# Kernel tuning notes

Measured on AMD Instinct MI355X. Metric: run time of the kernel, lower is better.

Reference implementation:

```python
import jax, jax.numpy as jnp
import numpy as np

# ---- config (matches init_kwargs) ----
L_LEVELS = 10          # int(log(8192/16)/log(2)) + 1
LEVEL_DIM = 4
BASE_RES = 16
LOG2_T = 21
BOUND = 2.0            # contract() output bound
DENSITY_BIAS = -1.0
RGB_PADDING = 0.001
DEG_VIEW = 4
PRIME1 = np.uint32(2654435761)
PRIME2 = np.uint32(805459861)


def _grid_meta():
    # torch-ngp GridEncoder layout: per-level scale = base*2^l - 1 (per_level_scale=2),
    # resolution = base*2^l, params = min(2^21, (res+1)^3) rounded up to multiple of 8.
    offsets, scales, res_list, sizes = [0], [], [], []
    for l in range(L_LEVELS):
        res = BASE_RES * (2 ** l)
        scales.append(float(res - 1))
        n = min(2 ** LOG2_T, (res + 1) ** 3)
        n = int(np.ceil(n / 8) * 8)
        res_list.append(res)
        sizes.append(n)
        offsets.append(offsets[-1] + n)
    return scales, res_list, sizes, offsets

GRID_SCALES, GRID_RES, GRID_SIZES, GRID_OFFSETS = _grid_meta()
TOTAL_PARAMS = GRID_OFFSETS[-1]  # 14995560
CORNERS = np.array([[(c >> d) & 1 for d in range(3)] for c in range(8)], dtype=np.int32)


def contract(x):
    # mipnerf360 contraction, output in [-2, 2]
    eps = jnp.finfo(x.dtype).eps
    x_mag_sq = jnp.maximum(eps, jnp.sum(x * x, axis=-1, keepdims=True))
    return jnp.where(x_mag_sq <= 1.0, x, ((2.0 * jnp.sqrt(x_mag_sq) - 1.0) / x_mag_sq) * x)


def pos_enc(x):
    # coord.pos_enc with identity, min_deg=0, max_deg=DEG_VIEW -> dim 3 + 3*2*4 = 27
    scales = 2.0 ** jnp.arange(DEG_VIEW, dtype=x.dtype)
    xb = (x[..., None, :] * scales[:, None]).reshape(x.shape[:-1] + (3 * DEG_VIEW,))
    four = jnp.sin(jnp.concatenate([xb, xb + 0.5 * jnp.pi], axis=-1))
    return jnp.concatenate([x, four], axis=-1)


def grid_encode(x01, embeddings):
    # x01: [N,3] in [0,1]; embeddings: [TOTAL_PARAMS, LEVEL_DIM]
    feats = []
    for l in range(L_LEVELS):
        pos = x01 * GRID_SCALES[l] + 0.5  # align_corners=False
        pos_floor = jnp.floor(pos)
        frac = pos - pos_floor            # trilinear weights, differentiable in x01
        pg = pos_floor.astype(jnp.int32)  # [N,3]
        res1 = GRID_RES[l] + 1
        size = GRID_SIZES[l]
        use_hash = (res1 ** 3) > size
        lvl_emb = embeddings[GRID_OFFSETS[l]:GRID_OFFSETS[l] + size]
        acc = jnp.zeros(x01.shape[:-1] + (LEVEL_DIM,), x01.dtype)
        for c in range(8):
            off = CORNERS[c]
            corner = pg + off[None, :]
            if use_hash:
                cu = corner.astype(jnp.uint32)
                idx = (cu[:, 0] ^ (cu[:, 1] * PRIME1) ^ (cu[:, 2] * PRIME2)) % jnp.uint32(size)
                idx = idx.astype(jnp.int32)
            else:
                idx = corner[:, 0] + corner[:, 1] * res1 + corner[:, 2] * (res1 * res1)
            w = jnp.prod(jnp.where(off[None, :] == 1, frac, 1.0 - frac), axis=-1)  # [N]
            acc = acc + w[:, None] * lvl_emb[idx]
        feats.append(acc)
    return jnp.concatenate(feats, axis=-1)  # [N, 40]


def setup_inputs() -> dict:
    key = jax.random.key(0)
    ks = jax.random.split(key, 10)
    R, S = 2048, 32
    coords = jax.random.normal(ks[0], (R, S, 3), jnp.float32) * 1.5
    viewdirs = jax.random.normal(ks[1], (R, 3), jnp.float32)
    viewdirs = viewdirs / jnp.linalg.norm(viewdirs, axis=-1, keepdims=True)
    embeddings = (jax.random.uniform(ks[2], (TOTAL_PARAMS, LEVEL_DIM), jnp.float32) * 2.0 - 1.0) * 1e-4

    def lin(k, fan_in, fan_out):
        k1, k2 = jax.random.split(k)
        lim = 1.0 / np.sqrt(fan_in)
        w = jax.random.uniform(k1, (fan_in, fan_out), jnp.float32, -lim, lim)
        b = jax.random.uniform(k2, (fan_out,), jnp.float32, -lim, lim)
        return w, b

    w_d1, b_d1 = lin(ks[3], L_LEVELS * LEVEL_DIM, 64)
    w_d2, b_d2 = lin(ks[4], 64, 256)
    DIR_DIM = 3 + 3 * 2 * DEG_VIEW  # 27
    w_r0, b_r0 = lin(ks[5], 256 + DIR_DIM, 256)          # 283 -> 256
    w_r1, b_r1 = lin(ks[6], 256 + 256 + DIR_DIM, 256)    # skip concat: 539 -> 256
    w_rgb, b_rgb = lin(ks[7], 256, 3)
    return dict(coords=coords, viewdirs=viewdirs, embeddings=embeddings,
                w_d1=w_d1, b_d1=b_d1, w_d2=w_d2, b_d2=b_d2,
                w_r0=w_r0, b_r0=b_r0, w_r1=w_r1, b_r1=b_r1,
                w_rgb=w_rgb, b_rgb=b_rgb)


def reference(coords, viewdirs, embeddings, w_d1, b_d1, w_d2, b_d2,
              w_r0, b_r0, w_r1, b_r1, w_rgb, b_rgb):
    shape = coords.shape[:-1]  # (rays, samples)
    cw = contract(coords) / BOUND          # coords_warped, in [-1, 1]
    x01 = (cw.reshape(-1, 3) + BOUND) / (2.0 * BOUND)  # encoder normalization with bound=2
    feats = grid_encode(x01, embeddings)               # [N, 40]
    h = jax.nn.relu(feats @ w_d1 + b_d1)
    x = h @ w_d2 + b_d2                                # [N, 256]
    raw_density = x[:, 0].reshape(shape)
    density = jax.nn.softplus(raw_density + DENSITY_BIAS)
    bottleneck = x.reshape(shape + (256,))
    dir_enc = pos_enc(viewdirs)                        # [rays, 27]
    dir_enc = jnp.broadcast_to(dir_enc[..., None, :], shape + (dir_enc.shape[-1],))
    inp = jnp.concatenate([bottleneck, dir_enc], axis=-1)  # [rays, S, 283]
    y = jax.nn.relu(inp @ w_r0 + b_r0)
    y = jnp.concatenate([y, inp], axis=-1)             # skip at layer i == skip_layer_dir == 0
    y = jax.nn.relu(y @ w_r1 + b_r1)
    rgb = jax.nn.sigmoid(y @ w_rgb + b_rgb)            # rgb_premultiplier=1, rgb_bias=0
    rgb = rgb * (1.0 + 2.0 * RGB_PADDING) - RGB_PADDING
    return cw, density, rgb
```

## Files before the change

kernel.cpp:

```cpp
#include <hip/hip_runtime.h>
#include <math.h>

#define NS 65536
#define NRAYS 2048

typedef __attribute__((ext_vector_type(8))) short short8;
typedef __attribute__((ext_vector_type(4))) float f32x4;
typedef unsigned short u16;

#define OFF_FEATS 0ull
#define OFF_HBF   10485760ull
#define OFF_XBF   18874368ull
#define OFF_DW0   85983232ull
#define OFF_DW1   88080384ull
#define OFF_WD2T  90177536ull
#define OFF_WR0T  90210304ull
#define OFF_WR1T  90341376ull

#define OUT_DENS 196608
#define OUT_RGB  262144

__device__ __forceinline__ u16 f2b(float f) {
    unsigned u = __builtin_bit_cast(unsigned, f);
    return (u16)((u + 0x7FFFu + ((u >> 16) & 1u)) >> 16);
}

__global__ __launch_bounds__(256) void cvt_weights(
    const float* __restrict__ w_d2, const float* __restrict__ w_r0,
    const float* __restrict__ w_r1, u16* __restrict__ wd2t,
    u16* __restrict__ wr0t, u16* __restrict__ wr1t)
{
    int idx = blockIdx.x * 256 + threadIdx.x;
    if (idx < 16384)  wd2t[idx] = f2b(w_d2[(idx & 63)  * 256 + (idx >> 6)]);
    if (idx < 65536)  wr0t[idx] = f2b(w_r0[(idx & 255) * 256 + (idx >> 8)]);
    if (idx < 131072) wr1t[idx] = f2b(w_r1[(idx & 511) * 256 + (idx >> 9)]);
}

__global__ __launch_bounds__(256) void dir_kernel(
    const float* __restrict__ viewdirs,
    const float* __restrict__ w_r0, const float* __restrict__ b_r0,
    const float* __restrict__ w_r1, const float* __restrict__ b_r1,
    float* __restrict__ dirW0, float* __restrict__ dirW1)
{
    __shared__ float de[27];
    int ray = blockIdx.x, t = threadIdx.x;
    if (t < 27) {
        float v;
        if (t < 3) v = viewdirs[3*ray + t];
        else {
            int k = (t - 3) % 12;
            float b = viewdirs[3*ray + (k % 3)] * (float)(1 << (k / 3));
            v = (t < 15) ? sinf(b) : sinf(b + 1.5707964f);
        }
        de[t] = v;
    }
    __syncthreads();
    float a0 = b_r0[t], a1 = b_r1[t];
#pragma unroll
    for (int d = 0; d < 27; ++d) {
        a0 = fmaf(de[d], w_r0[(256+d)*256 + t], a0);
        a1 = fmaf(de[d], w_r1[(512+d)*256 + t], a1);
    }
    dirW0[ray*256 + t] = a0;
    dirW1[ray*256 + t] = a1;
}

__global__ __launch_bounds__(256) void encode_kernel(
    const float* __restrict__ coords, const float* __restrict__ emb,
    float* __restrict__ cw_out, float* __restrict__ featsT)
{
    int t = threadIdx.x;
    int l = blockIdx.x >> 8;
    int i = ((blockIdx.x & 255) << 8) + t;
    float x = coords[3*i], y = coords[3*i+1], z = coords[3*i+2];
    float m2 = fmaxf(x*x + y*y + z*z, 1.1920928955078125e-07f);
    float cx = x, cy = y, cz = z;
    if (m2 > 1.0f) { float s = (2.0f*sqrtf(m2) - 1.0f)/m2; cx*=s; cy*=s; cz*=s; }
    cx *= 0.5f; cy *= 0.5f; cz *= 0.5f;
    if (l == 0) { cw_out[3*i]=cx; cw_out[3*i+1]=cy; cw_out[3*i+2]=cz; }
    float u0 = (cx + 2.0f)*0.25f, u1 = (cy + 2.0f)*0.25f, u2 = (cz + 2.0f)*0.25f;

    int res = 16 << l;
    int res1 = res + 1;
    float scale = (float)(res - 1);
    unsigned off = (l >= 3) ? 315496u + (unsigned)(l-3)*2097152u
                            : (l == 0 ? 0u : (l == 1 ? 4920u : 40864u));
    float p0 = u0*scale + 0.5f, p1 = u1*scale + 0.5f, p2 = u2*scale + 0.5f;
    float f0 = floorf(p0), f1 = floorf(p1), f2 = floorf(p2);
    float fr0 = p0-f0, fr1 = p1-f1, fr2 = p2-f2;
    unsigned g0 = (unsigned)(int)f0, g1 = (unsigned)(int)f1, g2 = (unsigned)(int)f2;
    float a0=0.f, a1=0.f, a2=0.f, a3=0.f;
    bool use_hash = (l >= 3);
#pragma unroll
    for (int c = 0; c < 8; ++c) {
        unsigned ox = c & 1u, oy = (c >> 1) & 1u, oz = (c >> 2) & 1u;
        unsigned qx = g0 + ox, qy = g1 + oy, qz = g2 + oz;
        unsigned idx;
        if (use_hash) idx = (qx ^ (qy*2654435761u) ^ (qz*805459861u)) & 2097151u;
        else          idx = qx + qy*(unsigned)res1 + qz*(unsigned)(res1*res1);
        const float4 e = *(const float4*)(emb + 4u*(off + idx));
        float w = (ox ? fr0 : 1.0f-fr0) * (oy ? fr1 : 1.0f-fr1) * (oz ? fr2 : 1.0f-fr2);
        a0 = fmaf(w, e.x, a0); a1 = fmaf(w, e.y, a1);
        a2 = fmaf(w, e.z, a2); a3 = fmaf(w, e.w, a3);
    }
    featsT[(4*l+0)*NS + i] = a0;
    featsT[(4*l+1)*NS + i] = a1;
    featsT[(4*l+2)*NS + i] = a2;
    featsT[(4*l+3)*NS + i] = a3;
}

__global__ __launch_bounds__(256) void gemm_d1_kernel(
    const float* __restrict__ featsT, const float* __restrict__ w_d1,
    const float* __restrict__ b_d1, const float* __restrict__ w_d2,
    const float* __restrict__ b_d2, u16* __restrict__ h_bf,
    float* __restrict__ dens)
{
    __shared__ float As[40][256];
    __shared__ float Ws[40*64];
    __shared__ float wc0[64];
    int t = threadIdx.x;
    int m0 = blockIdx.x * 256;
#pragma unroll
    for (int k = 0; k < 40; ++k) As[k][t] = featsT[k*NS + m0 + t];
#pragma unroll
    for (int i = 0; i < 10; ++i) Ws[i*256 + t] = w_d1[i*256 + t];
    if (t < 64) wc0[t] = w_d2[t*256];
    __syncthreads();
    int tn = t & 3, tm = t >> 2;
    float acc[4][16] = {};
#pragma unroll
    for (int k = 0; k < 40; ++k) {
        float4 a = *(const float4*)&As[k][tm*4];
        float av[4] = {a.x, a.y, a.z, a.w};
        const float4* wp = (const float4*)&Ws[k*64 + tn*16];
#pragma unroll
        for (int r = 0; r < 4; ++r) {
            float4 w = wp[r];
            float wv[4] = {w.x, w.y, w.z, w.w};
#pragma unroll
            for (int ii = 0; ii < 4; ++ii)
#pragma unroll
                for (int cc = 0; cc < 4; ++cc)
                    acc[ii][r*4+cc] = fmaf(av[ii], wv[cc], acc[ii][r*4+cc]);
        }
    }
    float p[4] = {0.f, 0.f, 0.f, 0.f};
#pragma unroll
    for (int jj = 0; jj < 16; ++jj) {
        int j = tn*16 + jj;
        float bj = b_d1[j], w0 = wc0[j];
#pragma unroll
        for (int ii = 0; ii < 4; ++ii) {
            float h = fmaxf(acc[ii][jj] + bj, 0.f);
            acc[ii][jj] = h;
            p[ii] = fmaf(h, w0, p[ii]);
        }
    }
#pragma unroll
    for (int ii = 0; ii < 4; ++ii) {
        int s = m0 + tm*4 + ii;
        unsigned u[8];
#pragma unroll
        for (int q = 0; q < 8; ++q)
            u[q] = (unsigned)f2b(acc[ii][2*q]) | ((unsigned)f2b(acc[ii][2*q+1]) << 16);
        uint4 v0 = {u[0], u[1], u[2], u[3]};
        uint4 v1 = {u[4], u[5], u[6], u[7]};
        *(uint4*)(h_bf + (size_t)s*64 + tn*16)     = v0;
        *(uint4*)(h_bf + (size_t)s*64 + tn*16 + 8) = v1;
    }
#pragma unroll
    for (int ii = 0; ii < 4; ++ii) {
        p[ii] += __shfl_xor(p[ii], 1, 64);
        p[ii] += __shfl_xor(p[ii], 2, 64);
    }
    if (tn == 0) {
        float b0 = b_d2[0];
#pragma unroll
        for (int ii = 0; ii < 4; ++ii) {
            float z = p[ii] + b0 - 1.0f;
            dens[m0 + tm*4 + ii] = fmaxf(z, 0.f) + log1pf(expf(-fabsf(z)));
        }
    }
}

#define MFMA __builtin_amdgcn_mfma_f32_16x16x32_bf16

__global__ __launch_bounds__(256) void mfma_d2(
    const u16* __restrict__ h_bf, const u16* __restrict__ wt,
    const float* __restrict__ b_d2, u16* __restrict__ xbf)
{
    __shared__ u16 xt[4][8192];
    int t = threadIdx.x, lane = t & 63, w = t >> 6;
    int m0 = blockIdx.x*128 + w*32;
    int rl = lane & 15, kg = (lane >> 4) * 8;
    f32x4 zero = {0.f,0.f,0.f,0.f};
    f32x4 acc[2][16];
#pragma unroll
    for (int a = 0; a < 2; ++a)
#pragma unroll
        for (int b = 0; b < 16; ++b) acc[a][b] = zero;
    const u16* pA0 = h_bf + (size_t)(m0 + rl)*64 + kg;
    const u16* pA1 = h_bf + (size_t)(m0 + 16 + rl)*64 + kg;
    const u16* pB  = wt + rl*64 + kg;
#pragma unroll
    for (int ks = 0; ks < 2; ++ks) {
        int kb = ks*32;
        short8 a0 = *(const short8*)(pA0 + kb);
        short8 a1 = *(const short8*)(pA1 + kb);
#pragma unroll
        for (int nt = 0; nt < 16; ++nt) {
            short8 b = *(const short8*)(pB + nt*1024 + kb);
            acc[0][nt] = MFMA(a0, b, acc[0][nt], 0, 0, 0);
            acc[1][nt] = MFMA(a1, b, acc[1][nt], 0, 0, 0);
        }
    }
    int ro = (lane >> 4) * 4;
    u16* xw = xt[w];
#pragma unroll
    for (int nt = 0; nt < 16; ++nt) {
        int col = nt*16 + rl;
        float bias = b_d2[col];
#pragma unroll
        for (int mt = 0; mt < 2; ++mt)
#pragma unroll
            for (int r = 0; r < 4; ++r) {
                int row = mt*16 + ro + r;
                unsigned byte = (unsigned)(row*512 + col*2) ^ ((unsigned)(row & 7) << 4);
                xw[byte >> 1] = f2b(acc[mt][nt][r] + bias);
            }
    }
#pragma unroll
    for (int it = 0; it < 16; ++it) {
        unsigned flat = it*1024u + (unsigned)lane*16u;
        unsigned row = flat >> 9, off = flat & 511u;
        unsigned lb = flat ^ ((row & 7u) << 4);
        short8 v = *(const short8*)((const char*)xw + lb);
        *(short8*)(xbf + (size_t)(m0 + row)*256 + (off >> 1)) = v;
    }
}

__global__ __launch_bounds__(256) void mfma_tail(
    const u16* __restrict__ xbf, const u16* __restrict__ w0t,
    const u16* __restrict__ w1t, const float* __restrict__ dirW0,
    const float* __restrict__ dirW1, const float* __restrict__ w_rgb,
    const float* __restrict__ b_rgb, float* __restrict__ rgb)
{
    __shared__ u16 yt[4][8192];
    int t = threadIdx.x, lane = t & 63, w = t >> 6;
    int m0 = blockIdx.x*128 + w*32;
    int rl = lane & 15, kg = (lane >> 4) * 8;
    int ro = (lane >> 4) * 4;
    f32x4 zero = {0.f,0.f,0.f,0.f};
    const u16* pA0 = xbf + (size_t)(m0 + rl)*256 + kg;
    const u16* pA1 = xbf + (size_t)(m0 + 16 + rl)*256 + kg;

    f32x4 acc0[2][16];
#pragma unroll
    for (int a = 0; a < 2; ++a)
#pragma unroll
        for (int b = 0; b < 16; ++b) acc0[a][b] = zero;
    {
        const u16* pB = w0t + rl*256 + kg;
#pragma unroll
        for (int ks = 0; ks < 8; ++ks) {
            int kb = ks*32;
            short8 a0 = *(const short8*)(pA0 + kb);
            short8 a1 = *(const short8*)(pA1 + kb);
#pragma unroll
            for (int nt = 0; nt < 16; ++nt) {
                short8 b = *(const short8*)(pB + nt*4096 + kb);
                acc0[0][nt] = MFMA(a0, b, acc0[0][nt], 0, 0, 0);
                acc0[1][nt] = MFMA(a1, b, acc0[1][nt], 0, 0, 0);
            }
        }
    }
    {
        const float* dir0 = dirW0 + (m0 >> 5)*256;
        u16* yw = yt[w];
#pragma unroll
        for (int nt = 0; nt < 16; ++nt) {
            int col = nt*16 + rl;
            float bias = dir0[col];
#pragma unroll
            for (int mt = 0; mt < 2; ++mt)
#pragma unroll
                for (int r = 0; r < 4; ++r) {
                    int row = mt*16 + ro + r;
                    unsigned byte = (unsigned)(row*512 + col*2) ^ ((unsigned)(row & 7) << 4);
                    yw[byte >> 1] = f2b(fmaxf(acc0[mt][nt][r] + bias, 0.f));
                }
        }
    }
    f32x4 acc1[2][16];
#pragma unroll
    for (int a = 0; a < 2; ++a)
#pragma unroll
        for (int b = 0; b < 16; ++b) acc1[a][b] = zero;
    {
        const u16* pB = w1t + rl*512;
        const char* ywc = (const char*)yt[w];
        unsigned sw = ((unsigned)(rl & 7)) << 4;
#pragma unroll
        for (int ks = 0; ks < 8; ++ks) {
            int kb = ks*32;
            unsigned base = (unsigned)((kb + kg)*2);
            short8 a0 = *(const short8*)(ywc + (((unsigned)(rl*512)       + base) ^ sw));
            short8 a1 = *(const short8*)(ywc + (((unsigned)((16+rl)*512)  + base) ^ sw));
#pragma unroll
            for (int nt = 0; nt < 16; ++nt) {
                short8 b = *(const short8*)(pB + nt*8192 + kg + kb);
                acc1[0][nt] = MFMA(a0, b, acc1[0][nt], 0, 0, 0);
                acc1[1][nt] = MFMA(a1, b, acc1[1][nt], 0, 0, 0);
            }
        }
#pragma unroll
        for (int ks = 8; ks < 16; ++ks) {
            int kb = ks*32;
            int kl = kb - 256;
            short8 a0 = *(const short8*)(pA0 + kl);
            short8 a1 = *(const short8*)(pA1 + kl);
#pragma unroll
            for (int nt = 0; nt < 16; ++nt) {
                short8 b = *(const short8*)(pB + nt*8192 + kg + kb);
                acc1[0][nt] = MFMA(a0, b, acc1[0][nt], 0, 0, 0);
                acc1[1][nt] = MFMA(a1, b, acc1[1][nt], 0, 0, 0);
            }
        }
    }
    const float* dir1 = dirW1 + (m0 >> 5)*256;
    float p[2][4][3];
#pragma unroll
    for (int mt = 0; mt < 2; ++mt)
#pragma unroll
        for (int r = 0; r < 4; ++r)
            p[mt][r][0] = p[mt][r][1] = p[mt][r][2] = 0.f;
#pragma unroll
    for (int nt = 0; nt < 16; ++nt) {
        int col = nt*16 + rl;
        float dv = dir1[col];
        float w0 = w_rgb[col*3], w1 = w_rgb[col*3+1], w2 = w_rgb[col*3+2];
#pragma unroll
        for (int mt = 0; mt < 2; ++mt)
#pragma unroll
            for (int r = 0; r < 4; ++r) {
                float y1 = fmaxf(acc1[mt][nt][r] + dv, 0.f);
                p[mt][r][0] = fmaf(y1, w0, p[mt][r][0]);
                p[mt][r][1] = fmaf(y1, w1, p[mt][r][1]);
                p[mt][r][2] = fmaf(y1, w2, p[mt][r][2]);
            }
    }
#pragma unroll
    for (int mask = 1; mask < 16; mask <<= 1)
#pragma unroll
        for (int mt = 0; mt < 2; ++mt)
#pragma unroll
            for (int r = 0; r < 4; ++r)
#pragma unroll
                for (int c = 0; c < 3; ++c)
                    p[mt][r][c] += __shfl_xor(p[mt][r][c], mask, 64);
    if (rl == 0) {
#pragma unroll
        for (int mt = 0; mt < 2; ++mt)
#pragma unroll
            for (int r = 0; r < 4; ++r) {
                int row = m0 + mt*16 + ro + r;
#pragma unroll
                for (int c = 0; c < 3; ++c) {
                    float v = p[mt][r][c] + b_rgb[c];
                    float sg = 1.0f / (1.0f + expf(-v));
                    rgb[row*3 + c] = sg * 1.002f - 0.001f;
                }
            }
    }
}

extern "C" void kernel_launch(void* const* d_in, const int* in_sizes, int n_in,
                              void* d_out, int out_size, void* d_ws, size_t ws_size,
                              hipStream_t stream)
{
    const float* coords   = (const float*)d_in[0];
    const float* viewdirs = (const float*)d_in[1];
    const float* emb      = (const float*)d_in[2];
    const float* w_d1     = (const float*)d_in[3];
    const float* b_d1     = (const float*)d_in[4];
    const float* w_d2     = (const float*)d_in[5];
    const float* b_d2     = (const float*)d_in[6];
    const float* w_r0     = (const float*)d_in[7];
    const float* b_r0     = (const float*)d_in[8];
    const float* w_r1     = (const float*)d_in[9];
    const float* b_r1     = (const float*)d_in[10];
    const float* w_rgb    = (const float*)d_in[11];
    const float* b_rgb    = (const float*)d_in[12];

    float* out  = (float*)d_out;
    float* cw   = out;
    float* dens = out + OUT_DENS;
    float* rgb  = out + OUT_RGB;

    char* wsB = (char*)d_ws;
    float* featsT = (float*)(wsB + OFF_FEATS);
    u16*   h_bf   = (u16*)(wsB + OFF_HBF);
    u16*   xbf    = (u16*)(wsB + OFF_XBF);
    float* dirW0  = (float*)(wsB + OFF_DW0);
    float* dirW1  = (float*)(wsB + OFF_DW1);
    u16*   wd2t   = (u16*)(wsB + OFF_WD2T);
    u16*   wr0t   = (u16*)(wsB + OFF_WR0T);
    u16*   wr1t   = (u16*)(wsB + OFF_WR1T);

    cvt_weights<<<512, 256, 0, stream>>>(w_d2, w_r0, w_r1, wd2t, wr0t, wr1t);
    dir_kernel<<<NRAYS, 256, 0, stream>>>(viewdirs, w_r0, b_r0, w_r1, b_r1, dirW0, dirW1);
    encode_kernel<<<2560, 256, 0, stream>>>(coords, emb, cw, featsT);
    gemm_d1_kernel<<<NS/256, 256, 0, stream>>>(featsT, w_d1, b_d1, w_d2, b_d2, h_bf, dens);
    mfma_d2<<<NS/128, 256, 0, stream>>>(h_bf, wd2t, b_d2, xbf);
    mfma_tail<<<NS/128, 256, 0, stream>>>(xbf, wr0t, wr1t, dirW0, dirW1, w_rgb, b_rgb, rgb);
}
```

Baseline: 495.5 us.

## Fuse d2 GEMM into tail kernel and keep bottleneck activations in registers

Measured after the change: 511.6 us. 3.3% more time.

```diff
diff --git a/kernel.cpp b/kernel.cpp
--- a/kernel.cpp
+++ b/kernel.cpp
@@ -10,7 +10,6 @@
 
 #define OFF_FEATS 0ull
 #define OFF_HBF   10485760ull
-#define OFF_XBF   18874368ull
 #define OFF_DW0   85983232ull
 #define OFF_DW1   88080384ull
 #define OFF_WD2T  90177536ull
@@ -185,98 +184,88 @@
 
 #define MFMA __builtin_amdgcn_mfma_f32_16x16x32_bf16
 
-__global__ __launch_bounds__(256) void mfma_d2(
-    const u16* __restrict__ h_bf, const u16* __restrict__ wt,
-    const float* __restrict__ b_d2, u16* __restrict__ xbf)
-{
-    __shared__ u16 xt[4][8192];
-    int t = threadIdx.x, lane = t & 63, w = t >> 6;
-    int m0 = blockIdx.x*128 + w*32;
-    int rl = lane & 15, kg = (lane >> 4) * 8;
-    f32x4 zero = {0.f,0.f,0.f,0.f};
-    f32x4 acc[2][16];
-#pragma unroll
-    for (int a = 0; a < 2; ++a)
-#pragma unroll
-        for (int b = 0; b < 16; ++b) acc[a][b] = zero;
-    const u16* pA0 = h_bf + (size_t)(m0 + rl)*64 + kg;
-    const u16* pA1 = h_bf + (size_t)(m0 + 16 + rl)*64 + kg;
-    const u16* pB  = wt + rl*64 + kg;
-#pragma unroll
-    for (int ks = 0; ks < 2; ++ks) {
-        int kb = ks*32;
-        short8 a0 = *(const short8*)(pA0 + kb);
-        short8 a1 = *(const short8*)(pA1 + kb);
-#pragma unroll
-        for (int nt = 0; nt < 16; ++nt) {
-            short8 b = *(const short8*)(pB + nt*1024 + kb);
-            acc[0][nt] = MFMA(a0, b, acc[0][nt], 0, 0, 0);
-            acc[1][nt] = MFMA(a1, b, acc[1][nt], 0, 0, 0);
-        }
-    }
-    int ro = (lane >> 4) * 4;
-    u16* xw = xt[w];
-#pragma unroll
-    for (int nt = 0; nt < 16; ++nt) {
-        int col = nt*16 + rl;
-        float bias = b_d2[col];
-#pragma unroll
-        for (int mt = 0; mt < 2; ++mt)
-#pragma unroll
-            for (int r = 0; r < 4; ++r) {
-                int row = mt*16 + ro + r;
-                unsigned byte = (unsigned)(row*512 + col*2) ^ ((unsigned)(row & 7) << 4);
-                xw[byte >> 1] = f2b(acc[mt][nt][r] + bias);
-            }
-    }
-#pragma unroll
-    for (int it = 0; it < 16; ++it) {
-        unsigned flat = it*1024u + (unsigned)lane*16u;
-        unsigned row = flat >> 9, off = flat & 511u;
-        unsigned lb = flat ^ ((row & 7u) << 4);
-        short8 v = *(const short8*)((const char*)xw + lb);
-        *(short8*)(xbf + (size_t)(m0 + row)*256 + (off >> 1)) = v;
-    }
-}
-
-__global__ __launch_bounds__(256) void mfma_tail(
-    const u16* __restrict__ xbf, const u16* __restrict__ w0t,
-    const u16* __restrict__ w1t, const float* __restrict__ dirW0,
+__global__ __launch_bounds__(256, 2) void mfma_tail(
+    const u16* __restrict__ h_bf, const u16* __restrict__ wd2t,
+    const u16* __restrict__ w0t, const u16* __restrict__ w1t,
+    const float* __restrict__ b_d2, const float* __restrict__ dirW0,
     const float* __restrict__ dirW1, const float* __restrict__ w_rgb,
     const float* __restrict__ b_rgb, float* __restrict__ rgb)
 {
-    __shared__ u16 yt[4][8192];
+    __shared__ u16 tile[4][8192];
     int t = threadIdx.x, lane = t & 63, w = t >> 6;
     int m0 = blockIdx.x*128 + w*32;
     int rl = lane & 15, kg = (lane >> 4) * 8;
     int ro = (lane >> 4) * 4;
     f32x4 zero = {0.f,0.f,0.f,0.f};
-    const u16* pA0 = xbf + (size_t)(m0 + rl)*256 + kg;
-    const u16* pA1 = xbf + (size_t)(m0 + 16 + rl)*256 + kg;
-
-    f32x4 acc0[2][16];
+    u16* tw = tile[w];
+    const char* twc = (const char*)tw;
+    unsigned swA = ((unsigned)(rl & 7)) << 4;
+
+    f32x4 acc[2][16];
+
 #pragma unroll
     for (int a = 0; a < 2; ++a)
 #pragma unroll
-        for (int b = 0; b < 16; ++b) acc0[a][b] = zero;
+        for (int b = 0; b < 16; ++b) acc[a][b] = zero;
     {
-        const u16* pB = w0t + rl*256 + kg;
-#pragma unroll
-        for (int ks = 0; ks < 8; ++ks) {
+        const u16* pA0 = h_bf + (size_t)(m0 + rl)*64 + kg;
+        const u16* pA1 = h_bf + (size_t)(m0 + 16 + rl)*64 + kg;
+        const u16* pB  = wd2t + rl*64 + kg;
+#pragma unroll
+        for (int ks = 0; ks < 2; ++ks) {
             int kb = ks*32;
             short8 a0 = *(const short8*)(pA0 + kb);
             short8 a1 = *(const short8*)(pA1 + kb);
 #pragma unroll
             for (int nt = 0; nt < 16; ++nt) {
+                short8 b = *(const short8*)(pB + nt*1024 + kb);
+                acc[0][nt] = MFMA(a0, b, acc[0][nt], 0, 0, 0);
+                acc[1][nt] = MFMA(a1, b, acc[1][nt], 0, 0, 0);
+            }
+        }
+    }
+#pragma unroll
+    for (int nt = 0; nt < 16; ++nt) {
+        int col = nt*16 + rl;
+        float bias = b_d2[col];
+#pragma unroll
+        for (int mt = 0; mt < 2; ++mt)
+#pragma unroll
+            for (int r = 0; r < 4; ++r) {
+                int row = mt*16 + ro + r;
+                unsigned byte = (unsigned)(row*512 + col*2) ^ ((unsigned)(row & 7) << 4);
+                tw[byte >> 1] = f2b(acc[mt][nt][r] + bias);
+            }
+    }
+    __syncthreads();
+    short8 xa0[8], xa1[8];
+#pragma unroll
+    for (int ks = 0; ks < 8; ++ks) {
+        unsigned base = (unsigned)((ks*32 + kg)*2);
+        xa0[ks] = *(const short8*)(twc + (((unsigned)(rl*512)      + base) ^ swA));
+        xa1[ks] = *(const short8*)(twc + (((unsigned)((16+rl)*512) + base) ^ swA));
+    }
+    __syncthreads();
+
+#pragma unroll
+    for (int a = 0; a < 2; ++a)
+#pragma unroll
+        for (int b = 0; b < 16; ++b) acc[a][b] = zero;
+    {
+        const u16* pB = w0t + rl*256 + kg;
+#pragma unroll
+        for (int ks = 0; ks < 8; ++ks) {
+            int kb = ks*32;
+#pragma unroll
+            for (int nt = 0; nt < 16; ++nt) {
                 short8 b = *(const short8*)(pB + nt*4096 + kb);
-                acc0[0][nt] = MFMA(a0, b, acc0[0][nt], 0, 0, 0);
-                acc0[1][nt] = MFMA(a1, b, acc0[1][nt], 0, 0, 0);
+                acc[0][nt] = MFMA(xa0[ks], b, acc[0][nt], 0, 0, 0);
+                acc[1][nt] = MFMA(xa1[ks], b, acc[1][nt], 0, 0, 0);
             }
         }
     }
     {
         const float* dir0 = dirW0 + (m0 >> 5)*256;
-        u16* yw = yt[w];
 #pragma unroll
         for (int nt = 0; nt < 16; ++nt) {
             int col = nt*16 + rl;
@@ -287,46 +276,43 @@
                 for (int r = 0; r < 4; ++r) {
                     int row = mt*16 + ro + r;
                     unsigned byte = (unsigned)(row*512 + col*2) ^ ((unsigned)(row & 7) << 4);
-                    yw[byte >> 1] = f2b(fmaxf(acc0[mt][nt][r] + bias, 0.f));
+                    tw[byte >> 1] = f2b(fmaxf(acc[mt][nt][r] + bias, 0.f));
                 }
         }
     }
-    f32x4 acc1[2][16];
+    __syncthreads();
+
 #pragma unroll
     for (int a = 0; a < 2; ++a)
 #pragma unroll
-        for (int b = 0; b < 16; ++b) acc1[a][b] = zero;
+        for (int b = 0; b < 16; ++b) acc[a][b] = zero;
     {
-        const u16* pB = w1t + rl*512;
-        const char* ywc = (const char*)yt[w];
-        unsigned sw = ((unsigned)(rl & 7)) << 4;
+        const u16* pB = w1t + rl*512 + kg;
+#pragma unroll
+        for (int ks = 0; ks < 8; ++ks) {
+            int kb = 256 + ks*32;
+#pragma unroll
+            for (int nt = 0; nt < 16; ++nt) {
+                short8 b = *(const short8*)(pB + nt*8192 + kb);
+                acc[0][nt] = MFMA(xa0[ks], b, acc[0][nt], 0, 0, 0);
+                acc[1][nt] = MFMA(xa1[ks], b, acc[1][nt], 0, 0, 0);
+            }
+        }
 #pragma unroll
         for (int ks = 0; ks < 8; ++ks) {
             int kb = ks*32;
             unsigned base = (unsigned)((kb + kg)*2);
-            short8 a0 = *(const short8*)(ywc + (((unsigned)(rl*512)       + base) ^ sw));
-            short8 a1 = *(const short8*)(ywc + (((unsigned)((16+rl)*512)  + base) ^ sw));
+            short8 ya0 = *(const short8*)(twc + (((unsigned)(rl*512)      + base) ^ swA));
+            short8 ya1 = *(const short8*)(twc + (((unsigned)((16+rl)*512) + base) ^ swA));
 #pragma unroll
             for (int nt = 0; nt < 16; ++nt) {
-                short8 b = *(const short8*)(pB + nt*8192 + kg + kb);
-                acc1[0][nt] = MFMA(a0, b, acc1[0][nt], 0, 0, 0);
-                acc1[1][nt] = MFMA(a1, b, acc1[1][nt], 0, 0, 0);
-            }
-        }
-#pragma unroll
-        for (int ks = 8; ks < 16; ++ks) {
-            int kb = ks*32;
-            int kl = kb - 256;
-            short8 a0 = *(const short8*)(pA0 + kl);
-            short8 a1 = *(const short8*)(pA1 + kl);
-#pragma unroll
-            for (int nt = 0; nt < 16; ++nt) {
-                short8 b = *(const short8*)(pB + nt*8192 + kg + kb);
-                acc1[0][nt] = MFMA(a0, b, acc1[0][nt], 0, 0, 0);
-                acc1[1][nt] = MFMA(a1, b, acc1[1][nt], 0, 0, 0);
-            }
-        }
-    }
+                short8 b = *(const short8*)(pB + nt*8192 + kb);
+                acc[0][nt] = MFMA(ya0, b, acc[0][nt], 0, 0, 0);
+                acc[1][nt] = MFMA(ya1, b, acc[1][nt], 0, 0, 0);
+            }
+        }
+    }
+
     const float* dir1 = dirW1 + (m0 >> 5)*256;
     float p[2][4][3];
 #pragma unroll
@@ -343,7 +329,7 @@
         for (int mt = 0; mt < 2; ++mt)
 #pragma unroll
             for (int r = 0; r < 4; ++r) {
-                float y1 = fmaxf(acc1[mt][nt][r] + dv, 0.f);
+                float y1 = fmaxf(acc[mt][nt][r] + dv, 0.f);
                 p[mt][r][0] = fmaf(y1, w0, p[mt][r][0]);
                 p[mt][r][1] = fmaf(y1, w1, p[mt][r][1]);
                 p[mt][r][2] = fmaf(y1, w2, p[mt][r][2]);
@@ -400,7 +386,6 @@
     char* wsB = (char*)d_ws;
     float* featsT = (float*)(wsB + OFF_FEATS);
     u16*   h_bf   = (u16*)(wsB + OFF_HBF);
-    u16*   xbf    = (u16*)(wsB + OFF_XBF);
     float* dirW0  = (float*)(wsB + OFF_DW0);
     float* dirW1  = (float*)(wsB + OFF_DW1);
     u16*   wd2t   = (u16*)(wsB + OFF_WD2T);
@@ -411,6 +396,6 @@
     dir_kernel<<<NRAYS, 256, 0, stream>>>(viewdirs, w_r0, b_r0, w_r1, b_r1, dirW0, dirW1);
     encode_kernel<<<2560, 256, 0, stream>>>(coords, emb, cw, featsT);
     gemm_d1_kernel<<<NS/256, 256, 0, stream>>>(featsT, w_d1, b_d1, w_d2, b_d2, h_bf, dens);
-    mfma_d2<<<NS/128, 256, 0, stream>>>(h_bf, wd2t, b_d2, xbf);
-    mfma_tail<<<NS/128, 256, 0, stream>>>(xbf, wr0t, wr1t, dirW0, dirW1, w_rgb, b_rgb, rgb);
-}
+    mfma_tail<<<NS/128, 256, 0, stream>>>(h_bf, wd2t, wr0t, wr1t, b_d2,
+                                          dirW0, dirW1, w_rgb, b_rgb, rgb);
+}
```
